# Optimization experiments

Measured on AMD Instinct MI355X. Metric: run time of the kernel, lower is better.

The kernel has to match this reference:

```python
import jax, jax.numpy as jnp
import numpy as np
import math

D_MODEL, D_INNER, D_STATE, D_CONV, DT_RANK = 768, 1536, 16, 4, 48
BATCH, SEQLEN = 2, 1024
DT_MIN, DT_MAX = 1e-4, 1.0


def setup_inputs() -> dict:
    key = jax.random.key(0)
    ks = jax.random.split(key, 10)
    D, N, R, K = D_INNER, D_STATE, DT_RANK, D_CONV
    total_out = 2 * D + R + 2 * D * N

    def xavier(k, shape):
        fan_in, fan_out = shape[1], shape[0]
        a = math.sqrt(6.0 / (fan_in + fan_out))
        return jax.random.uniform(k, shape, jnp.float32, -a, a)

    x = jax.random.normal(ks[0], (BATCH, SEQLEN, D_MODEL), jnp.float32)
    W_in = xavier(ks[1], (total_out, D_MODEL))
    W_dt = xavier(ks[2], (D, R))
    W_out = xavier(ks[3], (D_MODEL, D))
    W_res = xavier(ks[4], (D, D_MODEL))
    conv_w = jax.random.normal(ks[5], (D, K), jnp.float32) * (1.0 / math.sqrt(K))
    conv_b = jnp.zeros((D,), jnp.float32)
    # A_log init: log(1..N) per inner channel
    A_log = jnp.broadcast_to(jnp.log(jnp.arange(1, N + 1, dtype=jnp.float32)), (D, N))
    Dskip = jnp.ones((D,), jnp.float32)
    # dt_bias = inverse_softplus(exp(uniform in [log dt_min, log dt_max]))
    dt = jnp.exp(jax.random.uniform(ks[6], (D,), jnp.float32) * (math.log(DT_MAX) - math.log(DT_MIN)) + math.log(DT_MIN))
    dt_bias = dt + jnp.log(-jnp.expm1(-dt))
    norm_w = jnp.ones((D,), jnp.float32)
    ln_w = jnp.ones((D_MODEL,), jnp.float32)
    ln_b = jnp.zeros((D_MODEL,), jnp.float32)
    return {
        "x": x, "ln_w": ln_w, "ln_b": ln_b, "W_in": W_in, "W_dt": W_dt,
        "conv_w": conv_w, "conv_b": conv_b, "A_log": A_log, "Dskip": Dskip,
        "dt_bias": dt_bias, "norm_w": norm_w, "W_res": W_res, "W_out": W_out,
    }


def _forward(x, ln_w, ln_b, W_in, W_dt, conv_w, conv_b, A_log, Dskip, dt_bias, norm_w, W_res, W_out):
    B, L, _ = x.shape
    D, N = A_log.shape
    K = conv_w.shape[1]
    R = W_dt.shape[1]
    # pre LayerNorm
    mu = x.mean(-1, keepdims=True)
    var = ((x - mu) ** 2).mean(-1, keepdims=True)
    xn = (x - mu) * jax.lax.rsqrt(var + 1e-5) * ln_w + ln_b
    # fused input projection, then split
    p = jnp.einsum('bld,od->blo', xn, W_in)  # (B,L,2D+R+2DN)
    z = p[..., :D]
    u = p[..., D:2 * D]
    dth = p[..., 2 * D:2 * D + R]
    Bpar = p[..., 2 * D + R:2 * D + R + D * N].reshape(B, L, D, N)
    Cpar = p[..., 2 * D + R + D * N:].reshape(B, L, D, N)
    # causal depthwise conv over time on u
    uc = jax.lax.conv_general_dilated(
        u.transpose(0, 2, 1), conv_w[:, None, :], (1,), [(K - 1, 0)],
        feature_group_count=D, dimension_numbers=('NCH', 'OIH', 'NCH'))
    u = (uc + conv_b[None, :, None]).transpose(0, 2, 1)  # (B,L,D)
    # dt: low-rank proj + bias -> softplus -> clamp
    dt = jnp.clip(jax.nn.softplus(jnp.einsum('blr,dr->bld', dth, W_dt) + dt_bias), DT_MIN, DT_MAX)
    A = -jnp.exp(A_log)  # (D,N), negative
    dA = jnp.exp(dt[..., None] * A)          # (B,L,D,N)
    dBu = (dt * u)[..., None] * Bpar         # (B,L,D,N)

    def step(h, inp):
        dA_t, dBu_t, C_t = inp               # each (B,D,N)
        h = dA_t * h + dBu_t
        return h, (C_t * h).sum(-1)          # y_t: (B,D)

    h0 = jnp.zeros((B, D, N), x.dtype)
    _, ys = jax.lax.scan(step, h0, (dA.transpose(1, 0, 2, 3),
                                    dBu.transpose(1, 0, 2, 3),
                                    Cpar.transpose(1, 0, 2, 3)))
    y = ys.transpose(1, 0, 2) + u * Dskip    # (B,L,D)
    # fused gated RMSNorm + inner residual
    res = jnp.einsum('blm,dm->bld', x, W_res)
    g = y * jax.nn.silu(z)
    g = g * jax.lax.rsqrt((g * g).mean(-1, keepdims=True) + 1e-6) * norm_w + res
    return jnp.einsum('bld,md->blm', g, W_out)


def reference(x, ln_w, ln_b, W_in, W_dt, conv_w, conv_b, A_log, Dskip, dt_bias, norm_w, W_res, W_out):
    return _forward(x, ln_w, ln_b, W_in, W_dt, conv_w, conv_b, A_log, Dskip, dt_bias, norm_w, W_res, W_out)
```

## Files before the change

kernel.cpp:

```cpp
#include <hip/hip_runtime.h>


typedef unsigned short u16;
typedef __bf16 bf16x8 __attribute__((ext_vector_type(8)));
typedef float f32x4 __attribute__((ext_vector_type(4)));

#define OPAD 52480
#define OTOT 52272
#define DI   1536
#define DM   768
#define Z0   0
#define U0   1536
#define DTH0 3072
#define B0   3120
#define C0   27696

#define SCAN_P 64
#define SCAN_T 16
#define SPF    4

__device__ static inline u16 f2bf(float f) {
    unsigned u = __float_as_uint(f);
    u += 0x7fffu + ((u >> 16) & 1u);
    return (u16)(u >> 16);
}
__device__ static inline float bf2f(u16 s) {
    return __uint_as_float(((unsigned)s) << 16);
}

__device__ static inline void gload16(const void* g, void* l) {
    __builtin_amdgcn_global_load_lds(
        (const __attribute__((address_space(1))) unsigned int*)g,
        (__attribute__((address_space(3))) unsigned int*)l, 16, 0, 0);
}

__device__ static inline void unpack8(uint4 v, float* f) {
    unsigned w0 = v.x, w1 = v.y, w2 = v.z, w3 = v.w;
    f[0] = __uint_as_float(w0 << 16); f[1] = __uint_as_float(w0 & 0xffff0000u);
    f[2] = __uint_as_float(w1 << 16); f[3] = __uint_as_float(w1 & 0xffff0000u);
    f[4] = __uint_as_float(w2 << 16); f[5] = __uint_as_float(w2 & 0xffff0000u);
    f[6] = __uint_as_float(w3 << 16); f[7] = __uint_as_float(w3 & 0xffff0000u);
}

__global__ void cvt_kernel(const float* __restrict__ src, u16* __restrict__ dst,
                           long n_src, long n_tot) {
    long i4 = ((long)blockIdx.x * 256 + threadIdx.x) * 4;
    if (i4 >= n_tot) return;
    ushort4 o;
    if (i4 < n_src) {
        float4 v = *(const float4*)(src + i4);
        o.x = f2bf(v.x); o.y = f2bf(v.y); o.z = f2bf(v.z); o.w = f2bf(v.w);
    } else {
        o.x = o.y = o.z = o.w = 0;
    }
    *(ushort4*)(dst + i4) = o;
}

__device__ static inline void block_reduce2(float& a, float& b) {
    #pragma unroll
    for (int o = 32; o > 0; o >>= 1) {
        a += __shfl_down(a, o);
        b += __shfl_down(b, o);
    }
    __shared__ float sa[4], sb[4];
    int lane = threadIdx.x & 63, w = threadIdx.x >> 6;
    if (lane == 0) { sa[w] = a; sb[w] = b; }
    __syncthreads();
    a = sa[0] + sa[1] + sa[2] + sa[3];
    b = sb[0] + sb[1] + sb[2] + sb[3];
}

__global__ void __launch_bounds__(256) ln_kernel(const float* __restrict__ x,
        const float* __restrict__ w, const float* __restrict__ b,
        u16* __restrict__ xnbf, u16* __restrict__ xbf) {
    int m = blockIdx.x, tid = threadIdx.x;
    const float* xr = x + (size_t)m * DM;
    float v[3];
    v[0] = xr[tid]; v[1] = xr[tid + 256]; v[2] = xr[tid + 512];
    float s = v[0] + v[1] + v[2];
    float ss = v[0]*v[0] + v[1]*v[1] + v[2]*v[2];
    block_reduce2(s, ss);
    float mu = s * (1.f / DM);
    float var = ss * (1.f / DM) - mu * mu;
    float inv = rsqrtf(var + 1e-5f);
    #pragma unroll
    for (int i = 0; i < 3; ++i) {
        int d = tid + i * 256;
        float xn = (v[i] - mu) * inv * w[d] + b[d];
        xnbf[(size_t)m * DM + d] = f2bf(xn);
        xbf[(size_t)m * DM + d] = f2bf(v[i]);
    }
}

template <int OUT_BF16>
__global__ void __launch_bounds__(256) gemm_bt(const u16* __restrict__ A,
        const u16* __restrict__ B, void* __restrict__ C, int K, int ldc) {
    __shared__ u16 smem[2 * 128 * 64];
    u16* As = smem;
    u16* Bs = smem + 128 * 64;
    int tid = threadIdx.x;
    int m0 = blockIdx.x * 128, n0 = blockIdx.y * 128;
    int lane = tid & 63, wave = tid >> 6;
    int wm = wave >> 1, wn = wave & 1;
    int l15 = lane & 15, l4 = lane >> 4;
    f32x4 acc[4][4] = {};
    const u16* Ag = A + (size_t)m0 * K;
    const u16* Bg = B + (size_t)n0 * K;
    int crow = tid >> 3;
    int ccol = ((tid & 7) ^ ((tid >> 3) & 7)) * 8;
    int ldsoff = (tid & 192) * 16;
    int xr = l15 & 7;

    for (int k0 = 0; k0 < K; k0 += 64) {
        __syncthreads();
        #pragma unroll
        for (int it = 0; it < 4; ++it) {
            gload16(Ag + (size_t)(it * 32 + crow) * K + k0 + ccol,
                    (char*)As + it * 4096 + ldsoff);
            gload16(Bg + (size_t)(it * 32 + crow) * K + k0 + ccol,
                    (char*)Bs + it * 4096 + ldsoff);
        }
        __syncthreads();
        const u16* Arow = As + (wm * 64 + l15) * 64;
        const u16* Brow = Bs + (wn * 64 + l15) * 64;
        #pragma unroll
        for (int kk8 = 0; kk8 < 8; kk8 += 4) {
            int sw = ((l4 + kk8) ^ xr) * 8;
            bf16x8 af[4], bfr[4];
            #pragma unroll
            for (int i = 0; i < 4; ++i) af[i] = *(const bf16x8*)(Arow + i * 16 * 64 + sw);
            #pragma unroll
            for (int j = 0; j < 4; ++j) bfr[j] = *(const bf16x8*)(Brow + j * 16 * 64 + sw);
            #pragma unroll
            for (int i = 0; i < 4; ++i)
                #pragma unroll
                for (int j = 0; j < 4; ++j)
                    acc[i][j] = __builtin_amdgcn_mfma_f32_16x16x32_bf16(
                        af[i], bfr[j], acc[i][j], 0, 0, 0);
        }
    }
    #pragma unroll
    for (int i = 0; i < 4; ++i) {
        int row = m0 + wm * 64 + i * 16 + l4 * 4;
        #pragma unroll
        for (int j = 0; j < 4; ++j) {
            int col = n0 + wn * 64 + j * 16 + l15;
            #pragma unroll
            for (int r = 0; r < 4; ++r) {
                size_t off = (size_t)(row + r) * ldc + col;
                if (OUT_BF16) ((u16*)C)[off] = f2bf(acc[i][j][r]);
                else          ((float*)C)[off] = acc[i][j][r];
            }
        }
    }
}

#define G2_BUF  65536
#define G2_HALF 16384
#define G2_BOFF 32768

__global__ void __launch_bounds__(512, 2) gemm256_bt(const u16* __restrict__ A,
        const u16* __restrict__ B, u16* __restrict__ C, int K, int ldc) {
    __shared__ u16 smem[65536];
    char* smemc = (char*)smem;
    const int tid = threadIdx.x;
    const int l = tid & 63, w = tid >> 6;
    const int wm = w >> 2, wn = w & 3;
    const int l15 = l & 15, l4 = l >> 4;
    const int flat = blockIdx.y * 8 + blockIdx.x;
    const int wg = (flat & 7) * 205 + (flat >> 3);
    const int m0 = (wg & 7) * 256, n0 = (wg >> 3) * 256;
    const int NT = K >> 6;

    const int rA = l15 >> 1;
    const int rdoff = rA * 128 + ((((l4 << 1) + (l15 & 1)) ^ ((rA & 3) << 1)) << 4);
    const int wpr = (l & 7) ^ (((l >> 3) & 3) << 1);
    const int srow = w * 32 + ((l >> 3) << 1) + (wpr & 1);
    const u16* Ast = A + (size_t)(m0 + srow) * K + (wpr >> 1) * 8;
    const u16* Bst = B + (size_t)(n0 + srow) * K + (wpr >> 1) * 8;
    const int sdst = w * 2048;

    f32x4 acc[8][4] = {};
    bf16x8 bvK[4];

#define G2_STAGE(MATP, MOFF, nxt, sh, tk)                                      \
    gload16(MATP + (size_t)(tk) * 64 + (sh) * 32,                              \
            smemc + (nxt) * G2_BUF + (MOFF) + (sh) * G2_HALF + sdst);          \
    gload16(MATP + (size_t)16 * K + (size_t)(tk) * 64 + (sh) * 32,             \
            smemc + (nxt) * G2_BUF + (MOFF) + (sh) * G2_HALF + sdst + 1024);

#define G2_PHASE(cur, nxt, rh, h, READB, SMAT, SMOFF, sh, tk, DO_VM)           \
    {                                                                          \
        G2_STAGE(SMAT, SMOFF, nxt, sh, tk);                                    \
        const char* Ab = smemc + (cur) * G2_BUF + (h) * G2_HALF                \
                         + (wm * 128 + (rh) * 64) * 64 + rdoff;                \
        bf16x8 af[4];                                                          \
        if (READB) {                                                           \
            const char* Bb = smemc + (cur) * G2_BUF + G2_BOFF + (h) * G2_HALF  \
                             + (wn * 64) * 64 + rdoff;                         \
            _Pragma("unroll")                                                  \
            for (int j = 0; j < 4; ++j)                                        \
                bvK[j] = *(const bf16x8*)(Bb + j * 1024);                      \
        }                                                                      \
        _Pragma("unroll")                                                      \
        for (int i = 0; i < 4; ++i) af[i] = *(const bf16x8*)(Ab + i * 1024);   \
        __builtin_amdgcn_s_barrier();                                          \
        __builtin_amdgcn_s_setprio(1);                                         \
        _Pragma("unroll")                                                      \
        for (int i = 0; i < 4; ++i)                                            \
            _Pragma("unroll")                                                  \
            for (int j = 0; j < 4; ++j)                                        \
                acc[(rh) * 4 + i][j] = __builtin_amdgcn_mfma_f32_16x16x32_bf16(\
                    af[i], bvK[j], acc[(rh) * 4 + i][j], 0, 0, 0);             \
        __builtin_amdgcn_s_setprio(0);                                         \
        if (DO_VM) asm volatile("s_waitcnt vmcnt(4)" ::: "memory");            \
        __builtin_amdgcn_s_barrier();                                          \
    }

#define G2_TILE(cur, nxt, tk)                                                  \
    G2_PHASE(cur, nxt, 0, 0, 1, Ast, 0,       0, tk, 0)                        \
    G2_PHASE(cur, nxt, 1, 0, 0, Bst, G2_BOFF, 0, tk, 1)                        \
    G2_PHASE(cur, nxt, 0, 1, 1, Ast, 0,       1, tk, 0)                        \
    G2_PHASE(cur, nxt, 1, 1, 0, Bst, G2_BOFF, 1, tk, 1)

    G2_STAGE(Ast, 0,       0, 0, 0);
    G2_STAGE(Bst, G2_BOFF, 0, 0, 0);
    G2_STAGE(Ast, 0,       0, 1, 0);
    G2_STAGE(Bst, G2_BOFF, 0, 1, 0);
    asm volatile("s_waitcnt vmcnt(4)" ::: "memory");
    __builtin_amdgcn_s_barrier();

    for (int t = 0; t < NT; t += 2) {
        int tk1 = t + 1;
        int tk2 = (t + 2 < NT) ? t + 2 : NT - 1;
        G2_TILE(0, 1, tk1)
        G2_TILE(1, 0, tk2)
    }

    #pragma unroll
    for (int ai = 0; ai < 8; ++ai) {
        int row = m0 + wm * 128 + ai * 16 + l4 * 4;
        #pragma unroll
        for (int j = 0; j < 4; ++j) {
            int col = n0 + wn * 64 + j * 16 + l15;
            #pragma unroll
            for (int r = 0; r < 4; ++r)
                C[(size_t)(row + r) * ldc + col] = f2bf(acc[ai][j][r]);
        }
    }
#undef G2_STAGE
#undef G2_PHASE
#undef G2_TILE
}

__global__ void __launch_bounds__(256) dt_kernel(const u16* __restrict__ p,
        const float* __restrict__ Wdt, const float* __restrict__ dt_bias,
        float* __restrict__ dt) {
    int m0 = blockIdx.x * 16, tid = threadIdx.x;
    __shared__ float dth_s[16 * 48];
    for (int i = tid; i < 16 * 48; i += 256)
        dth_s[i] = bf2f(p[(size_t)(m0 + i / 48) * OPAD + DTH0 + (i % 48)]);
    __syncthreads();
    #pragma unroll
    for (int ii = 0; ii < 6; ++ii) {
        int d = ii * 256 + tid;
        float base = dt_bias[d];
        float acc[16];
        #pragma unroll
        for (int mm = 0; mm < 16; ++mm) acc[mm] = base;
        for (int r = 0; r < 48; ++r) {
            float wv = Wdt[d * 48 + r];
            #pragma unroll
            for (int mm = 0; mm < 16; ++mm)
                acc[mm] = fmaf(wv, dth_s[mm * 48 + r], acc[mm]);
        }
        #pragma unroll
        for (int mm = 0; mm < 16; ++mm) {
            float xv = acc[mm];
            float sp = xv > 20.f ? xv : log1pf(__expf(xv));
            sp = fminf(fmaxf(sp, 1e-4f), 1.0f);
            dt[(size_t)(m0 + mm) * DI + d] = sp;
        }
    }
}

__global__ void __launch_bounds__(256, 2) scan1_kernel(const u16* __restrict__ p,
        const float* __restrict__ dt, const float* __restrict__ A_log,
        const float* __restrict__ cw, const float* __restrict__ cb,
        float* __restrict__ chkA, float* __restrict__ chkB) {
    int d = blockIdx.x * 256 + threadIdx.x;
    int b = blockIdx.y, c = blockIdx.z;
    int t0base = c * SCAN_T;
    float a[16];
    #pragma unroll
    for (int n = 0; n < 16; ++n) a[n] = -__expf(A_log[d * 16 + n]);
    float cw0 = cw[d*4], cw1 = cw[d*4+1], cw2 = cw[d*4+2], cw3 = cw[d*4+3];
    float cbv = cb[d];
    const u16* pB = p + (size_t)(b * 1024 + t0base) * OPAD + B0 + d * 16;
    const u16* pU = p + (size_t)(b * 1024 + t0base) * OPAD + U0 + d;
    const float* dtp = dt + (size_t)(b * 1024 + t0base) * DI + d;
    float x1, x2, x3;
    if (c == 0) { x1 = x2 = x3 = 0.f; }
    else {
        x1 = bf2f(*(pU - (long)OPAD));
        x2 = bf2f(*(pU - 2L * OPAD));
        x3 = bf2f(*(pU - 3L * OPAD));
    }
    uint4 Br[SPF][2]; float dtr[SPF], xur[SPF];
    #pragma unroll
    for (int i = 0; i < SPF; ++i) {
        Br[i][0] = *(const uint4*)(pB + (size_t)i * OPAD);
        Br[i][1] = *(const uint4*)(pB + (size_t)i * OPAD + 8);
        dtr[i] = dtp[(size_t)i * DI];
        xur[i] = bf2f(pU[(size_t)i * OPAD]);
    }
    float h[16], Av[16];
    #pragma unroll
    for (int n = 0; n < 16; ++n) { h[n] = 0.f; Av[n] = 1.f; }
    for (int t0 = 0; t0 < SCAN_T; t0 += SPF) {
        #pragma unroll
        for (int s = 0; s < SPF; ++s) {
            int t = t0 + s;
            uint4 b0 = Br[s][0], b1 = Br[s][1];
            float dtv = dtr[s], xt = xur[s];
            int tl = t + SPF < SCAN_T ? t + SPF : SCAN_T - 1;
            Br[s][0] = *(const uint4*)(pB + (size_t)tl * OPAD);
            Br[s][1] = *(const uint4*)(pB + (size_t)tl * OPAD + 8);
            dtr[s] = dtp[(size_t)tl * DI];
            xur[s] = bf2f(pU[(size_t)tl * OPAD]);
            float uv = cbv;
            uv = fmaf(cw0, x3, uv);
            uv = fmaf(cw1, x2, uv);
            uv = fmaf(cw2, x1, uv);
            uv = fmaf(cw3, xt, uv);
            x3 = x2; x2 = x1; x1 = xt;
            float Bf[16];
            unpack8(b0, Bf); unpack8(b1, Bf + 8);
            float dtu = dtv * uv;
            #pragma unroll
            for (int n = 0; n < 16; ++n) {
                float dA = __expf(dtv * a[n]);
                h[n] = fmaf(dA, h[n], dtu * Bf[n]);
                Av[n] *= dA;
            }
        }
    }
    size_t o = (((size_t)c * 2 + b) * 1536 + d) * 16;
    #pragma unroll
    for (int k = 0; k < 4; ++k) {
        *(float4*)(chkA + o + k * 4) = make_float4(Av[4*k], Av[4*k+1], Av[4*k+2], Av[4*k+3]);
        *(float4*)(chkB + o + k * 4) = make_float4(h[4*k], h[4*k+1], h[4*k+2], h[4*k+3]);
    }
}

__global__ void __launch_bounds__(256) scan_comb_kernel(const float* __restrict__ chkA,
        const float* __restrict__ chkB, float* __restrict__ hstart) {
    int idx = blockIdx.x * 256 + threadIdx.x;
    float hs = 0.f;
    for (int c = 0; c < SCAN_P; ++c) {
        size_t o = (size_t)c * 49152 + idx;
        hstart[o] = hs;
        hs = fmaf(chkA[o], hs, chkB[o]);
    }
}

__global__ void __launch_bounds__(256, 2) scan2_kernel(const u16* __restrict__ p,
        const float* __restrict__ dt, const float* __restrict__ A_log,
        const float* __restrict__ cw, const float* __restrict__ cb,
        const float* __restrict__ Dskip,
        const float* __restrict__ hstart, float* __restrict__ y) {
    int d = blockIdx.x * 256 + threadIdx.x;
    int b = blockIdx.y, c = blockIdx.z;
    int t0base = c * SCAN_T;
    float a[16];
    #pragma unroll
    for (int n = 0; n < 16; ++n) a[n] = -__expf(A_log[d * 16 + n]);
    float Dsk = Dskip[d];
    float cw0 = cw[d*4], cw1 = cw[d*4+1], cw2 = cw[d*4+2], cw3 = cw[d*4+3];
    float cbv = cb[d];
    const u16* pB = p + (size_t)(b * 1024 + t0base) * OPAD + B0 + d * 16;
    const u16* pC = p + (size_t)(b * 1024 + t0base) * OPAD + C0 + d * 16;
    const u16* pU = p + (size_t)(b * 1024 + t0base) * OPAD + U0 + d;
    const float* dtp = dt + (size_t)(b * 1024 + t0base) * DI + d;
    float* yp        = y  + (size_t)(b * 1024 + t0base) * DI + d;
    float x1, x2, x3;
    if (c == 0) { x1 = x2 = x3 = 0.f; }
    else {
        x1 = bf2f(*(pU - (long)OPAD));
        x2 = bf2f(*(pU - 2L * OPAD));
        x3 = bf2f(*(pU - 3L * OPAD));
    }
    uint4 Br[SPF][2], Cr[SPF][2]; float dtr[SPF], xur[SPF];
    #pragma unroll
    for (int i = 0; i < SPF; ++i) {
        Br[i][0] = *(const uint4*)(pB + (size_t)i * OPAD);
        Br[i][1] = *(const uint4*)(pB + (size_t)i * OPAD + 8);
        Cr[i][0] = *(const uint4*)(pC + (size_t)i * OPAD);
        Cr[i][1] = *(const uint4*)(pC + (size_t)i * OPAD + 8);
        dtr[i] = dtp[(size_t)i * DI];
        xur[i] = bf2f(pU[(size_t)i * OPAD]);
    }
    float h[16];
    {
        size_t o = ((size_t)c * 3072 + (size_t)b * 1536 + d) * 16;
        #pragma unroll
        for (int k = 0; k < 4; ++k) {
            float4 hv = *(const float4*)(hstart + o + k * 4);
            h[4*k] = hv.x; h[4*k+1] = hv.y; h[4*k+2] = hv.z; h[4*k+3] = hv.w;
        }
    }
    for (int t0 = 0; t0 < SCAN_T; t0 += SPF) {
        #pragma unroll
        for (int s = 0; s < SPF; ++s) {
            int t = t0 + s;
            uint4 b0 = Br[s][0], b1 = Br[s][1], c0 = Cr[s][0], c1 = Cr[s][1];
            float dtv = dtr[s], xt = xur[s];
            int tl = t + SPF < SCAN_T ? t + SPF : SCAN_T - 1;
            Br[s][0] = *(const uint4*)(pB + (size_t)tl * OPAD);
            Br[s][1] = *(const uint4*)(pB + (size_t)tl * OPAD + 8);
            Cr[s][0] = *(const uint4*)(pC + (size_t)tl * OPAD);
            Cr[s][1] = *(const uint4*)(pC + (size_t)tl * OPAD + 8);
            dtr[s] = dtp[(size_t)tl * DI];
            xur[s] = bf2f(pU[(size_t)tl * OPAD]);
            float uv = cbv;
            uv = fmaf(cw0, x3, uv);
            uv = fmaf(cw1, x2, uv);
            uv = fmaf(cw2, x1, uv);
            uv = fmaf(cw3, xt, uv);
            x3 = x2; x2 = x1; x1 = xt;
            float Bf[16], Cf[16];
            unpack8(b0, Bf); unpack8(b1, Bf + 8);
            unpack8(c0, Cf); unpack8(c1, Cf + 8);
            float dtu = dtv * uv;
            #pragma unroll
            for (int n = 0; n < 16; ++n) {
                float dA = __expf(dtv * a[n]);
                h[n] = fmaf(dA, h[n], dtu * Bf[n]);
            }
            float a0 = fmaf(Cf[0], h[0], uv * Dsk), a1 = Cf[1] * h[1];
            float a2 = Cf[2] * h[2], a3 = Cf[3] * h[3];
            #pragma unroll
            for (int n = 4; n < 16; n += 4) {
                a0 = fmaf(Cf[n],   h[n],   a0);
                a1 = fmaf(Cf[n+1], h[n+1], a1);
                a2 = fmaf(Cf[n+2], h[n+2], a2);
                a3 = fmaf(Cf[n+3], h[n+3], a3);
            }
            yp[(size_t)t * DI] = (a0 + a1) + (a2 + a3);
        }
    }
}

__global__ void __launch_bounds__(256) gate_kernel(const u16* __restrict__ p,
        const float* __restrict__ y, const float* __restrict__ res,
        const float* __restrict__ norm_w, u16* __restrict__ g) {
    int m = blockIdx.x, tid = threadIdx.x;
    const u16* pz = p + (size_t)m * OPAD + Z0;
    const float* yr = y + (size_t)m * DI;
    float gp[6];
    float ss = 0.f, dummy = 0.f;
    #pragma unroll
    for (int i = 0; i < 6; ++i) {
        int d = i * 256 + tid;
        float z = bf2f(pz[d]);
        float gv = yr[d] * z / (1.f + __expf(-z));
        gp[i] = gv;
        ss += gv * gv;
    }
    block_reduce2(ss, dummy);
    float scale = rsqrtf(ss * (1.f / DI) + 1e-6f);
    #pragma unroll
    for (int i = 0; i < 6; ++i) {
        int d = i * 256 + tid;
        float val = gp[i] * scale * norm_w[d] + res[(size_t)m * DI + d];
        g[(size_t)m * DI + d] = f2bf(val);
    }
}

extern "C" void kernel_launch(void* const* d_in, const int* in_sizes, int n_in,
                              void* d_out, int out_size, void* d_ws, size_t ws_size,
                              hipStream_t stream) {
    const float* x       = (const float*)d_in[0];
    const float* ln_w    = (const float*)d_in[1];
    const float* ln_b    = (const float*)d_in[2];
    const float* W_in    = (const float*)d_in[3];
    const float* W_dt    = (const float*)d_in[4];
    const float* conv_w  = (const float*)d_in[5];
    const float* conv_b  = (const float*)d_in[6];
    const float* A_log   = (const float*)d_in[7];
    const float* Dskip   = (const float*)d_in[8];
    const float* dt_bias = (const float*)d_in[9];
    const float* norm_w  = (const float*)d_in[10];
    const float* W_res   = (const float*)d_in[11];
    const float* W_out   = (const float*)d_in[12];
    float* out = (float*)d_out;

    char* wsb = (char*)d_ws;
    u16* Wbf     = (u16*)(wsb + 0);
    u16* Wresbf  = (u16*)(wsb + 80609280);
    u16* Woutbf  = (u16*)(wsb + 82968576);
    u16* xnbf    = (u16*)(wsb + 85327872);
    u16* xbf     = (u16*)(wsb + 88473600);
    u16* pbuf    = (u16*)(wsb + 91619328);
    float* dtv   = (float*)(wsb + 319160320);
    float* ybuf  = (float*)(wsb + 331743232);
    float* resb  = (float*)(wsb + 344326144);
    u16* gbuf    = (u16*)(wsb + 356909056);
    float* chkA  = (float*)(wsb + 0);
    float* chkB  = (float*)(wsb + 12582912);
    float* hst   = (float*)(wsb + 25165824);

    cvt_kernel<<<39360, 256, 0, stream>>>(W_in, Wbf, (long)OTOT * DM, (long)OPAD * DM);
    cvt_kernel<<<1152, 256, 0, stream>>>(W_res, Wresbf, (long)DI * DM, (long)DI * DM);
    cvt_kernel<<<1152, 256, 0, stream>>>(W_out, Woutbf, (long)DM * DI, (long)DM * DI);
    ln_kernel<<<2048, 256, 0, stream>>>(x, ln_w, ln_b, xnbf, xbf);
    gemm256_bt<<<dim3(8, 205), 512, 0, stream>>>(xnbf, Wbf, pbuf, DM, OPAD);
    gemm_bt<0><<<dim3(16, 12), 256, 0, stream>>>(xbf, Wresbf, resb, DM, DI);
    dt_kernel<<<128, 256, 0, stream>>>(pbuf, W_dt, dt_bias, dtv);
    scan1_kernel<<<dim3(6, 2, SCAN_P), 256, 0, stream>>>(pbuf, dtv, A_log, conv_w, conv_b, chkA, chkB);
    scan_comb_kernel<<<192, 256, 0, stream>>>(chkA, chkB, hst);
    scan2_kernel<<<dim3(6, 2, SCAN_P), 256, 0, stream>>>(pbuf, dtv, A_log, conv_w, conv_b, Dskip, hst, ybuf);
    gate_kernel<<<2048, 256, 0, stream>>>(pbuf, ybuf, resb, norm_w, gbuf);
    gemm_bt<0><<<dim3(16, 6), 256, 0, stream>>>(gbuf, Woutbf, out, DI, DM);
}
```

Before: 691.4 us.

## Fuse prep kernels, split-K small GEMMs with atomics, shrink dt tiles, use exp2

Four independent changes. The three weight-conversion launches and the LayerNorm launch are merged into one prep kernel to cut launch overhead. The residual and output GEMMs become split-K (2 and 4 slices) that accumulate with atomicAdd into buffers zeroed by memset, which raises the block count on grids that were too small to fill the GPU. The dt kernel now handles 4 rows per block instead of 16, giving 512 blocks, and the scan kernels fold log2(e) into A so they can call exp2f. The costs are extra memsets, atomic traffic, and nondeterministic float summation order.

Measured after the change: 693.9 us. No clear change (+0.4%).

```diff
diff --git a/kernel.cpp b/kernel.cpp
--- a/kernel.cpp
+++ b/kernel.cpp
@@ -19,6 +19,8 @@
 #define SCAN_T 16
 #define SPF    4
 
+#define LOG2E 1.442695040888963f
+
 __device__ static inline u16 f2bf(float f) {
     unsigned u = __float_as_uint(f);
     u += 0x7fffu + ((u >> 16) & 1u);
@@ -42,20 +44,6 @@
     f[6] = __uint_as_float(w3 << 16); f[7] = __uint_as_float(w3 & 0xffff0000u);
 }
 
-__global__ void cvt_kernel(const float* __restrict__ src, u16* __restrict__ dst,
-                           long n_src, long n_tot) {
-    long i4 = ((long)blockIdx.x * 256 + threadIdx.x) * 4;
-    if (i4 >= n_tot) return;
-    ushort4 o;
-    if (i4 < n_src) {
-        float4 v = *(const float4*)(src + i4);
-        o.x = f2bf(v.x); o.y = f2bf(v.y); o.z = f2bf(v.z); o.w = f2bf(v.w);
-    } else {
-        o.x = o.y = o.z = o.w = 0;
-    }
-    *(ushort4*)(dst + i4) = o;
-}
-
 __device__ static inline void block_reduce2(float& a, float& b) {
     #pragma unroll
     for (int o = 32; o > 0; o >>= 1) {
@@ -70,31 +58,59 @@
     b = sb[0] + sb[1] + sb[2] + sb[3];
 }
 
-__global__ void __launch_bounds__(256) ln_kernel(const float* __restrict__ x,
-        const float* __restrict__ w, const float* __restrict__ b,
+__global__ void __launch_bounds__(256) prep_kernel(
+        const float* __restrict__ W_in, const float* __restrict__ W_res,
+        const float* __restrict__ W_out, const float* __restrict__ x,
+        const float* __restrict__ lnw, const float* __restrict__ lnb,
+        u16* __restrict__ Wbf, u16* __restrict__ Wresbf, u16* __restrict__ Woutbf,
         u16* __restrict__ xnbf, u16* __restrict__ xbf) {
-    int m = blockIdx.x, tid = threadIdx.x;
-    const float* xr = x + (size_t)m * DM;
-    float v[3];
-    v[0] = xr[tid]; v[1] = xr[tid + 256]; v[2] = xr[tid + 512];
-    float s = v[0] + v[1] + v[2];
-    float ss = v[0]*v[0] + v[1]*v[1] + v[2]*v[2];
-    block_reduce2(s, ss);
-    float mu = s * (1.f / DM);
-    float var = ss * (1.f / DM) - mu * mu;
-    float inv = rsqrtf(var + 1e-5f);
-    #pragma unroll
-    for (int i = 0; i < 3; ++i) {
-        int d = tid + i * 256;
-        float xn = (v[i] - mu) * inv * w[d] + b[d];
-        xnbf[(size_t)m * DM + d] = f2bf(xn);
-        xbf[(size_t)m * DM + d] = f2bf(v[i]);
-    }
-}
-
-template <int OUT_BF16>
+    int bid = blockIdx.x, tid = threadIdx.x;
+    if (bid < 41664) {
+        const float* src; u16* dst; long n_src, n_tot; long lb;
+        if (bid < 39360) {
+            src = W_in; dst = Wbf; n_src = (long)OTOT * DM; n_tot = (long)OPAD * DM;
+            lb = bid;
+        } else if (bid < 40512) {
+            src = W_res; dst = Wresbf; n_src = (long)DI * DM; n_tot = n_src;
+            lb = bid - 39360;
+        } else {
+            src = W_out; dst = Woutbf; n_src = (long)DM * DI; n_tot = n_src;
+            lb = bid - 40512;
+        }
+        long i4 = (lb * 256 + tid) * 4;
+        if (i4 >= n_tot) return;
+        ushort4 o;
+        if (i4 < n_src) {
+            float4 v = *(const float4*)(src + i4);
+            o.x = f2bf(v.x); o.y = f2bf(v.y); o.z = f2bf(v.z); o.w = f2bf(v.w);
+        } else {
+            o.x = o.y = o.z = o.w = 0;
+        }
+        *(ushort4*)(dst + i4) = o;
+    } else {
+        int m = bid - 41664;
+        const float* xr = x + (size_t)m * DM;
+        float v[3];
+        v[0] = xr[tid]; v[1] = xr[tid + 256]; v[2] = xr[tid + 512];
+        float s = v[0] + v[1] + v[2];
+        float ss = v[0]*v[0] + v[1]*v[1] + v[2]*v[2];
+        block_reduce2(s, ss);
+        float mu = s * (1.f / DM);
+        float var = ss * (1.f / DM) - mu * mu;
+        float inv = rsqrtf(var + 1e-5f);
+        #pragma unroll
+        for (int i = 0; i < 3; ++i) {
+            int d = tid + i * 256;
+            float xn = (v[i] - mu) * inv * lnw[d] + lnb[d];
+            xnbf[(size_t)m * DM + d] = f2bf(xn);
+            xbf[(size_t)m * DM + d] = f2bf(v[i]);
+        }
+    }
+}
+
+template <int OUT_BF16, int ATOMIC>
 __global__ void __launch_bounds__(256) gemm_bt(const u16* __restrict__ A,
-        const u16* __restrict__ B, void* __restrict__ C, int K, int ldc) {
+        const u16* __restrict__ B, void* __restrict__ C, int K, int ldk, int ldc) {
     __shared__ u16 smem[2 * 128 * 64];
     u16* As = smem;
     u16* Bs = smem + 128 * 64;
@@ -104,8 +120,8 @@
     int wm = wave >> 1, wn = wave & 1;
     int l15 = lane & 15, l4 = lane >> 4;
     f32x4 acc[4][4] = {};
-    const u16* Ag = A + (size_t)m0 * K;
-    const u16* Bg = B + (size_t)n0 * K;
+    const u16* Ag = A + (size_t)m0 * ldk + (size_t)blockIdx.z * K;
+    const u16* Bg = B + (size_t)n0 * ldk + (size_t)blockIdx.z * K;
     int crow = tid >> 3;
     int ccol = ((tid & 7) ^ ((tid >> 3) & 7)) * 8;
     int ldsoff = (tid & 192) * 16;
@@ -115,9 +131,9 @@
         __syncthreads();
         #pragma unroll
         for (int it = 0; it < 4; ++it) {
-            gload16(Ag + (size_t)(it * 32 + crow) * K + k0 + ccol,
+            gload16(Ag + (size_t)(it * 32 + crow) * ldk + k0 + ccol,
                     (char*)As + it * 4096 + ldsoff);
-            gload16(Bg + (size_t)(it * 32 + crow) * K + k0 + ccol,
+            gload16(Bg + (size_t)(it * 32 + crow) * ldk + k0 + ccol,
                     (char*)Bs + it * 4096 + ldsoff);
         }
         __syncthreads();
@@ -148,8 +164,9 @@
             #pragma unroll
             for (int r = 0; r < 4; ++r) {
                 size_t off = (size_t)(row + r) * ldc + col;
-                if (OUT_BF16) ((u16*)C)[off] = f2bf(acc[i][j][r]);
-                else          ((float*)C)[off] = acc[i][j][r];
+                if (ATOMIC)        atomicAdd((float*)C + off, acc[i][j][r]);
+                else if (OUT_BF16) ((u16*)C)[off] = f2bf(acc[i][j][r]);
+                else               ((float*)C)[off] = acc[i][j][r];
             }
         }
     }
@@ -256,26 +273,26 @@
 __global__ void __launch_bounds__(256) dt_kernel(const u16* __restrict__ p,
         const float* __restrict__ Wdt, const float* __restrict__ dt_bias,
         float* __restrict__ dt) {
-    int m0 = blockIdx.x * 16, tid = threadIdx.x;
-    __shared__ float dth_s[16 * 48];
-    for (int i = tid; i < 16 * 48; i += 256)
+    int m0 = blockIdx.x * 4, tid = threadIdx.x;
+    __shared__ float dth_s[4 * 48];
+    for (int i = tid; i < 4 * 48; i += 256)
         dth_s[i] = bf2f(p[(size_t)(m0 + i / 48) * OPAD + DTH0 + (i % 48)]);
     __syncthreads();
     #pragma unroll
     for (int ii = 0; ii < 6; ++ii) {
         int d = ii * 256 + tid;
         float base = dt_bias[d];
-        float acc[16];
-        #pragma unroll
-        for (int mm = 0; mm < 16; ++mm) acc[mm] = base;
+        float acc[4];
+        #pragma unroll
+        for (int mm = 0; mm < 4; ++mm) acc[mm] = base;
         for (int r = 0; r < 48; ++r) {
             float wv = Wdt[d * 48 + r];
             #pragma unroll
-            for (int mm = 0; mm < 16; ++mm)
+            for (int mm = 0; mm < 4; ++mm)
                 acc[mm] = fmaf(wv, dth_s[mm * 48 + r], acc[mm]);
         }
         #pragma unroll
-        for (int mm = 0; mm < 16; ++mm) {
+        for (int mm = 0; mm < 4; ++mm) {
             float xv = acc[mm];
             float sp = xv > 20.f ? xv : log1pf(__expf(xv));
             sp = fminf(fmaxf(sp, 1e-4f), 1.0f);
@@ -293,7 +310,7 @@
     int t0base = c * SCAN_T;
     float a[16];
     #pragma unroll
-    for (int n = 0; n < 16; ++n) a[n] = -__expf(A_log[d * 16 + n]);
+    for (int n = 0; n < 16; ++n) a[n] = -__expf(A_log[d * 16 + n]) * LOG2E;
     float cw0 = cw[d*4], cw1 = cw[d*4+1], cw2 = cw[d*4+2], cw3 = cw[d*4+3];
     float cbv = cb[d];
     const u16* pB = p + (size_t)(b * 1024 + t0base) * OPAD + B0 + d * 16;
@@ -339,7 +356,7 @@
             float dtu = dtv * uv;
             #pragma unroll
             for (int n = 0; n < 16; ++n) {
-                float dA = __expf(dtv * a[n]);
+                float dA = exp2f(dtv * a[n]);
                 h[n] = fmaf(dA, h[n], dtu * Bf[n]);
                 Av[n] *= dA;
             }
@@ -374,7 +391,7 @@
     int t0base = c * SCAN_T;
     float a[16];
     #pragma unroll
-    for (int n = 0; n < 16; ++n) a[n] = -__expf(A_log[d * 16 + n]);
+    for (int n = 0; n < 16; ++n) a[n] = -__expf(A_log[d * 16 + n]) * LOG2E;
     float Dsk = Dskip[d];
     float cw0 = cw[d*4], cw1 = cw[d*4+1], cw2 = cw[d*4+2], cw3 = cw[d*4+3];
     float cbv = cb[d];
@@ -434,7 +451,7 @@
             float dtu = dtv * uv;
             #pragma unroll
             for (int n = 0; n < 16; ++n) {
-                float dA = __expf(dtv * a[n]);
+                float dA = exp2f(dtv * a[n]);
                 h[n] = fmaf(dA, h[n], dtu * Bf[n]);
             }
             float a0 = fmaf(Cf[0], h[0], uv * Dsk), a1 = Cf[1] * h[1];
@@ -510,16 +527,16 @@
     float* chkB  = (float*)(wsb + 12582912);
     float* hst   = (float*)(wsb + 25165824);
 
-    cvt_kernel<<<39360, 256, 0, stream>>>(W_in, Wbf, (long)OTOT * DM, (long)OPAD * DM);
-    cvt_kernel<<<1152, 256, 0, stream>>>(W_res, Wresbf, (long)DI * DM, (long)DI * DM);
-    cvt_kernel<<<1152, 256, 0, stream>>>(W_out, Woutbf, (long)DM * DI, (long)DM * DI);
-    ln_kernel<<<2048, 256, 0, stream>>>(x, ln_w, ln_b, xnbf, xbf);
+    prep_kernel<<<43712, 256, 0, stream>>>(W_in, W_res, W_out, x, ln_w, ln_b,
+                                           Wbf, Wresbf, Woutbf, xnbf, xbf);
     gemm256_bt<<<dim3(8, 205), 512, 0, stream>>>(xnbf, Wbf, pbuf, DM, OPAD);
-    gemm_bt<0><<<dim3(16, 12), 256, 0, stream>>>(xbf, Wresbf, resb, DM, DI);
-    dt_kernel<<<128, 256, 0, stream>>>(pbuf, W_dt, dt_bias, dtv);
+    hipMemsetAsync(resb, 0, 12582912, stream);
+    gemm_bt<0, 1><<<dim3(16, 12, 2), 256, 0, stream>>>(xbf, Wresbf, resb, 384, DM, DI);
+    dt_kernel<<<512, 256, 0, stream>>>(pbuf, W_dt, dt_bias, dtv);
     scan1_kernel<<<dim3(6, 2, SCAN_P), 256, 0, stream>>>(pbuf, dtv, A_log, conv_w, conv_b, chkA, chkB);
     scan_comb_kernel<<<192, 256, 0, stream>>>(chkA, chkB, hst);
     scan2_kernel<<<dim3(6, 2, SCAN_P), 256, 0, stream>>>(pbuf, dtv, A_log, conv_w, conv_b, Dskip, hst, ybuf);
     gate_kernel<<<2048, 256, 0, stream>>>(pbuf, ybuf, resb, norm_w, gbuf);
-    gemm_bt<0><<<dim3(16, 6), 256, 0, stream>>>(gbuf, Woutbf, out, DI, DM);
-}
+    hipMemsetAsync(out, 0, (size_t)2048 * DM * 4, stream);
+    gemm_bt<0, 1><<<dim3(16, 6, 4), 256, 0, stream>>>(gbuf, Woutbf, out, 384, DI, DM);
+}
```
